# Kernel optimization log

Hardware: AMD Instinct MI355X
Metric: run time of the kernel (lower is better)

Reference implementation:

```python
import jax, jax.numpy as jnp
import numpy as np

B, S, D, H = 2, 2048, 1024, 16
DEPTH = D // H


def setup_inputs() -> dict:
    key = jax.random.key(0)
    ks = jax.random.split(key, 6)
    q = jax.random.normal(ks[0], (B, S, D), dtype=jnp.float32)
    k = jax.random.normal(ks[1], (B, S, D), dtype=jnp.float32)
    v = jax.random.normal(ks[2], (B, S, D), dtype=jnp.float32)
    # causal mask, broadcastable to [B, H, S, S]
    mask = jnp.tril(jnp.ones((S, S), dtype=bool))[None, None, :, :]
    wq = jax.random.normal(ks[3], (D, D), dtype=jnp.float32)
    wk = jax.random.normal(ks[4], (D, D), dtype=jnp.float32)
    wv = jax.random.normal(ks[5], (D, D), dtype=jnp.float32)
    return {"q": q, "k": k, "v": v, "mask": mask, "wq": wq, "wk": wk, "wv": wv}


def _split_heads(x):
    # [B, S, D] -> [B, H, S, depth]
    return x.reshape(x.shape[0], -1, H, DEPTH).transpose(0, 2, 1, 3)


def reference(q, k, v, mask, wq, wk, wv):
    q = _split_heads(q @ wq)
    k = _split_heads(k @ wk)
    v = _split_heads(v @ wv)
    scale = jnp.sqrt(jnp.float32(DEPTH))
    # [B, H, S, S]
    scores = jnp.einsum("bhqd,bhkd->bhqk", q, k) / scale
    scores = jnp.where(mask, scores, jnp.float32(-8.0))
    scores = scores - jnp.max(scores, axis=-1, keepdims=True)
    attn = jax.nn.softmax(scores, axis=-1)
    out = jnp.einsum("bhqk,bhkd->bhqd", attn, v)
    # [B, H, S, depth] -> [B, S, D]
    return out.transpose(0, 2, 1, 3).reshape(out.shape[0], -1, D)
```

## Files before the change

kernel.cpp:

```cpp
#include <hip/hip_runtime.h>
#include <hip/hip_bf16.h>

#define B_  2
#define S_  2048
#define D_  1024
#define H_  16
#define DH_ 64

typedef __attribute__((ext_vector_type(8)))  short  short8;
typedef __attribute__((ext_vector_type(4)))  short  short4b;
typedef __attribute__((ext_vector_type(16))) float  f32x16;

#define MFMA32(A,B,C) __builtin_amdgcn_mfma_f32_32x32x16_bf16(A,B,C,0,0,0)

static __device__ __forceinline__ short bf16b(float x) {
    __hip_bfloat16 h = __float2bfloat16(x);
    return *(short*)&h;
}
static __device__ __forceinline__ float bf16tof(short s) {
    union { unsigned u; float f; } cv;
    cv.u = ((unsigned)(unsigned short)s) << 16;
    return cv.f;
}
static __device__ __forceinline__ void gl2lds(const short* g, short* l) {
    __builtin_amdgcn_global_load_lds(
        (const __attribute__((address_space(1))) unsigned int*)g,
        (__attribute__((address_space(3))) unsigned int*)l, 16, 0, 0);
}

__global__ __launch_bounds__(256)
void conv_x(const float* __restrict__ q, const float* __restrict__ k,
            const float* __restrict__ v, char* __restrict__ ws) {
    const int z = blockIdx.y;
    const float* src = z == 0 ? q : z == 1 ? k : v;
    short* hi = (short*)(ws + (size_t)z * 16777216);
    short* lo = hi + 4194304;
    const int i = (blockIdx.x * 256 + threadIdx.x) * 4;
    float4 xv = *(const float4*)&src[i];
    const float* xf = (const float*)&xv;
    short4b h4, l4;
#pragma unroll
    for (int e = 0; e < 4; ++e) {
        short hb = bf16b(xf[e]);
        h4[e] = hb;
        l4[e] = bf16b(xf[e] - bf16tof(hb));
    }
    *(short4b*)&hi[i] = h4;
    *(short4b*)&lo[i] = l4;
}

__global__ __launch_bounds__(256)
void conv_wT(const float* __restrict__ wq, const float* __restrict__ wk,
             const float* __restrict__ wv, char* __restrict__ ws) {
    __shared__ short HiT[64][80];
    __shared__ short LoT[64][80];
    const int z = blockIdx.z;
    const float* w = z == 0 ? wq : z == 1 ? wk : wv;
    short* oh = (short*)(ws + 50331648 + (size_t)z * 4194304);
    short* ol = oh + 1048576;
    const int t  = threadIdx.x;
    const int k0 = blockIdx.x * 64, n0 = blockIdx.y * 64;

    const int kr = t >> 2, c4 = (t & 3) * 16;
    const float* srow = w + (size_t)(k0 + kr) * 1024 + n0 + c4;
#pragma unroll
    for (int u = 0; u < 16; u += 4) {
        float4 f = *(const float4*)&srow[u];
        const float* ff = (const float*)&f;
#pragma unroll
        for (int e = 0; e < 4; ++e) {
            int nl = c4 + u + e;
            short hb = bf16b(ff[e]);
            HiT[nl][kr] = hb;
            LoT[nl][kr] = bf16b(ff[e] - bf16tof(hb));
        }
    }
    __syncthreads();
    const int nl = t >> 2, kc = (t & 3) * 16;
    size_t off = (size_t)(n0 + nl) * 1024 + k0 + kc;
    *(short8*)&oh[off]     = *(const short8*)&HiT[nl][kc];
    *(short8*)&oh[off + 8] = *(const short8*)&HiT[nl][kc + 8];
    *(short8*)&ol[off]     = *(const short8*)&LoT[nl][kc];
    *(short8*)&ol[off + 8] = *(const short8*)&LoT[nl][kc + 8];
}

#define AHI_ 0
#define ALO_ 4096
#define BHI_ 8192
#define BLO_ 12288

__global__ __launch_bounds__(256, 2)
void proj_mfma(const short* __restrict__ xh0, const short* __restrict__ xl0,
               const short* __restrict__ xh1, const short* __restrict__ xl1,
               const short* __restrict__ xh2, const short* __restrict__ xl2,
               const short* __restrict__ wh0, const short* __restrict__ wl0,
               const short* __restrict__ wh1, const short* __restrict__ wl1,
               const short* __restrict__ wh2, const short* __restrict__ wl2,
               short* __restrict__ qh, short* __restrict__ ql,
               short* __restrict__ kh, short* __restrict__ kl,
               short* __restrict__ vt) {
    __shared__ short lds[16384];
    const int z  = blockIdx.z;
    const int m0 = blockIdx.y * 128;
    const int n0 = blockIdx.x * 128;
    const int t = threadIdx.x, lane = t & 63, w = t >> 6;
    const int l31 = lane & 31, hh = lane >> 5;

    const short* xh = z == 0 ? xh0 : z == 1 ? xh1 : xh2;
    const short* xl = z == 0 ? xl0 : z == 1 ? xl1 : xl2;
    const short* wh = z == 0 ? wh0 : z == 1 ? wh1 : wh2;
    const short* wl = z == 0 ? wl0 : z == 1 ? wl1 : wl2;

    const short* gsrc[8];
    short*       ldst[8];
#pragma unroll
    for (int j = 0; j < 8; ++j) {
        int sub = ((j & 1) << 2) | w;
        int cc  = (sub << 6) | lane;
        int row = cc >> 2, p = cc & 3;
        int kc  = p ^ ((row & 3) ^ ((row >> 2) & 3));
        bool isA  = j < 4;
        bool isHi = (j & 2) == 0;
        const short* base = isA ? (isHi ? xh : xl) : (isHi ? wh : wl);
        int r0g = isA ? m0 : n0;
        gsrc[j] = base + (size_t)(r0g + row) * 1024 + kc * 8;
        ldst[j] = &lds[(j >> 1) * 4096 + sub * 512];
    }

    const int rm0 = ((w & 1) << 6) + l31, rm1 = rm0 + 32;
    const int rn0 = ((w >> 1) << 6) + l31, rn1 = rn0 + 32;
    const int swm = (rm0 & 3) ^ ((rm0 >> 2) & 3);
    const int swn = (rn0 & 3) ^ ((rn0 >> 2) & 3);

    f32x16 accs[2][2] = {};

    for (int kt = 0; kt < 32; ++kt) {
        __syncthreads();
#pragma unroll
        for (int j = 0; j < 8; ++j)
            gl2lds(gsrc[j] + kt * 32, ldst[j]);
        __syncthreads();
#pragma unroll
        for (int ks = 0; ks < 2; ++ks) {
            const int kc = (ks << 1) | hh;
            const int om = (kc ^ swm) << 3;
            const int on = (kc ^ swn) << 3;
            short8 ah0 = *(const short8*)&lds[AHI_ + rm0 * 32 + om];
            short8 ah1 = *(const short8*)&lds[AHI_ + rm1 * 32 + om];
            short8 al0 = *(const short8*)&lds[ALO_ + rm0 * 32 + om];
            short8 al1 = *(const short8*)&lds[ALO_ + rm1 * 32 + om];
            short8 bh0 = *(const short8*)&lds[BHI_ + rn0 * 32 + on];
            short8 bh1 = *(const short8*)&lds[BHI_ + rn1 * 32 + on];
            short8 bl0 = *(const short8*)&lds[BLO_ + rn0 * 32 + on];
            short8 bl1 = *(const short8*)&lds[BLO_ + rn1 * 32 + on];
            accs[0][0] = MFMA32(ah0, bh0, accs[0][0]);
            accs[0][0] = MFMA32(ah0, bl0, accs[0][0]);
            accs[0][0] = MFMA32(al0, bh0, accs[0][0]);
            accs[0][1] = MFMA32(ah0, bh1, accs[0][1]);
            accs[0][1] = MFMA32(ah0, bl1, accs[0][1]);
            accs[0][1] = MFMA32(al0, bh1, accs[0][1]);
            accs[1][0] = MFMA32(ah1, bh0, accs[1][0]);
            accs[1][0] = MFMA32(ah1, bl0, accs[1][0]);
            accs[1][0] = MFMA32(al1, bh0, accs[1][0]);
            accs[1][1] = MFMA32(ah1, bh1, accs[1][1]);
            accs[1][1] = MFMA32(ah1, bl1, accs[1][1]);
            accs[1][1] = MFMA32(al1, bh1, accs[1][1]);
        }
    }

    const int qm = w & 1, qn = w >> 1;
    const int bb = m0 >> 11;
    const int sbase = (m0 & 2047) + qm * 64;
    if (z < 2) {
        short* oh = z == 0 ? qh : kh;
        short* ol = z == 0 ? ql : kl;
#pragma unroll
        for (int mt = 0; mt < 2; ++mt)
#pragma unroll
        for (int nt = 0; nt < 2; ++nt) {
            int n_g = n0 + qn * 64 + nt * 32 + l31;
            int h = n_g >> 6, d = n_g & 63;
#pragma unroll
            for (int r = 0; r < 16; ++r) {
                int s = sbase + mt * 32 + (r & 3) + 8 * (r >> 2) + 4 * hh;
                size_t off = (((size_t)(bb * 16 + h) * 2048 + s) << 6) + d;
                float a = accs[mt][nt][r];
                short hb = bf16b(a);
                oh[off] = hb;
                ol[off] = bf16b(a - bf16tof(hb));
            }
        }
    } else {
#pragma unroll
        for (int mt = 0; mt < 2; ++mt)
#pragma unroll
        for (int nt = 0; nt < 2; ++nt) {
            int n_g = n0 + qn * 64 + nt * 32 + l31;
            int h = n_g >> 6, d = n_g & 63;
            size_t vbase = ((size_t)(bb * 16 + h) * 64 + d) * 2048;
#pragma unroll
            for (int r2 = 0; r2 < 4; ++r2) {
                int s0 = sbase + mt * 32 + 8 * r2 + 4 * hh;
                short4b pk;
#pragma unroll
                for (int a2 = 0; a2 < 4; ++a2)
                    pk[a2] = bf16b(accs[mt][nt][r2 * 4 + a2]);
                *(short4b*)&vt[vbase + s0] = pk;
            }
        }
    }
}

__global__ void vtile_sums(const short* __restrict__ Vt, float* __restrict__ TS) {
    int c = blockIdx.x, bh = blockIdx.y, d = threadIdx.x;
    const short* row = Vt + ((size_t)bh * DH_ + d) * S_ + c * 64;
    float s = 0.f;
    for (int j = 0; j < 64; ++j) s += bf16tof(row[j]);
    TS[((size_t)bh * 32 + c) * 64 + d] = s;
}

__global__ void suffix_scan(const float* __restrict__ TS, float* __restrict__ SV) {
    int bh = blockIdx.x, d = threadIdx.x;
    float run = 0.f;
    for (int c = 32; c >= 0; --c) {
        SV[((size_t)bh * 33 + c) * 64 + d] = run;
        if (c > 0) run += TS[((size_t)bh * 32 + (c - 1)) * 64 + d];
    }
}

__global__ __launch_bounds__(256, 2)
void attn_mfma(const short* __restrict__ Qhi, const short* __restrict__ Qlo,
               const short* __restrict__ Khi, const short* __restrict__ Klo,
               const short* __restrict__ Vt,  const float* __restrict__ SV,
               float* __restrict__ out) {
    __shared__ __align__(16) short KhiS[64 * 72];
    __shared__ __align__(16) short KloS[64 * 72];
    __shared__ __align__(16) short VtS [64 * 72];
    __shared__ __align__(16) short PS  [4][32 * 72];

    const int t     = threadIdx.x;
    const int lane  = t & 63;
    const int w     = t >> 6;
    const int l31   = lane & 31;
    const int hh    = lane >> 5;
    const int bh    = blockIdx.x;
    const int yy    = blockIdx.y;
    const int qt    = (yy < 8) ? yy : 23 - yy;
    const int q0    = qt * 128;
    const int myq   = q0 + w * 32 + l31;
    const int ktend = 2 * qt + 2;

    const size_t basebh = (size_t)bh * S_ * DH_;

    short8 qh[4], ql[4];
    {
        const short* qr = Qhi + basebh + (size_t)myq * DH_;
        const short* lr = Qlo + basebh + (size_t)myq * DH_;
#pragma unroll
        for (int kf = 0; kf < 4; ++kf) {
            int dofs = kf * 16 + hh * 8;
            qh[kf] = *(const short8*)(qr + dofs);
            ql[kf] = *(const short8*)(lr + dofs);
        }
    }

    float m_run = -INFINITY, l_run = 0.f;
    f32x16 oT0 = {}, oT1 = {};

    const int srow = t >> 2;
    const int sc16 = (t & 3) * 16;

    for (int kt = 0; kt < ktend; ++kt) {
        __syncthreads();
        {
            const short* gH = Khi + basebh + (size_t)(kt * 64 + srow) * 64 + sc16;
            const short* gL = Klo + basebh + (size_t)(kt * 64 + srow) * 64 + sc16;
            const short* gV = Vt + (size_t)bh * DH_ * S_ + (size_t)srow * S_ + kt * 64 + sc16;
            short8 a0 = *(const short8*)gH, a1 = *(const short8*)(gH + 8);
            short8 b0 = *(const short8*)gL, b1 = *(const short8*)(gL + 8);
            short8 c0 = *(const short8*)gV, c1 = *(const short8*)(gV + 8);
            *(short8*)&KhiS[srow * 72 + sc16]     = a0;
            *(short8*)&KhiS[srow * 72 + sc16 + 8] = a1;
            *(short8*)&KloS[srow * 72 + sc16]     = b0;
            *(short8*)&KloS[srow * 72 + sc16 + 8] = b1;
            *(short8*)&VtS [srow * 72 + sc16]     = c0;
            *(short8*)&VtS [srow * 72 + sc16 + 8] = c1;
        }
        __syncthreads();

        f32x16 acc0 = {}, acc1 = {};
#pragma unroll
        for (int kf = 0; kf < 4; ++kf) {
            int dofs = kf * 16 + hh * 8;
            short8 k0h = *(const short8*)&KhiS[(l31)      * 72 + dofs];
            short8 k0l = *(const short8*)&KloS[(l31)      * 72 + dofs];
            short8 k1h = *(const short8*)&KhiS[(l31 + 32) * 72 + dofs];
            short8 k1l = *(const short8*)&KloS[(l31 + 32) * 72 + dofs];
            acc0 = MFMA32(k0h, qh[kf], acc0);
            acc0 = MFMA32(k0h, ql[kf], acc0);
            acc0 = MFMA32(k0l, qh[kf], acc0);
            acc1 = MFMA32(k1h, qh[kf], acc1);
            acc1 = MFMA32(k1h, ql[kf], acc1);
            acc1 = MFMA32(k1l, qh[kf], acc1);
        }

        float vals[32];
        float tmax = -INFINITY;
#pragma unroll
        for (int r = 0; r < 16; ++r) {
            int key0 = kt * 64 + ((r & 3) + 8 * (r >> 2) + 4 * hh);
            float v0 = acc0[r] * 0.125f;
            v0 = (key0 <= myq) ? v0 : -8.0f;
            float v1 = acc1[r] * 0.125f;
            v1 = (key0 + 32 <= myq) ? v1 : -8.0f;
            vals[r] = v0;
            vals[16 + r] = v1;
            tmax = fmaxf(tmax, fmaxf(v0, v1));
        }
        tmax = fmaxf(tmax, __shfl_xor(tmax, 32, 64));
        float mnew  = fmaxf(m_run, tmax);
        float alpha = __expf(m_run - mnew);
        float psum  = 0.f;
#pragma unroll
        for (int mt = 0; mt < 2; ++mt)
#pragma unroll
            for (int b2 = 0; b2 < 4; ++b2) {
                short4b pk;
#pragma unroll
                for (int a = 0; a < 4; ++a) {
                    float p = __expf(vals[mt * 16 + b2 * 4 + a] - mnew);
                    short pb = bf16b(p);
                    psum += bf16tof(pb);
                    pk[a] = pb;
                }
                *(short4b*)&PS[w][l31 * 72 + mt * 32 + b2 * 8 + hh * 4] = pk;
            }
        psum += __shfl_xor(psum, 32, 64);
        l_run = l_run * alpha + psum;
        m_run = mnew;
#pragma unroll
        for (int r = 0; r < 16; ++r) { oT0[r] *= alpha; oT1[r] *= alpha; }

#pragma unroll
        for (int kf = 0; kf < 4; ++kf) {
            int kofs = kf * 16 + hh * 8;
            short8 pf = *(const short8*)&PS[w][l31 * 72 + kofs];
            short8 v0 = *(const short8*)&VtS[(l31)      * 72 + kofs];
            short8 v1 = *(const short8*)&VtS[(l31 + 32) * 72 + kofs];
            oT0 = MFMA32(v0, pf, oT0);
            oT1 = MFMA32(v1, pf, oT1);
        }
    }

    {
        float mfin = fmaxf(m_run, -8.0f);
        float aa   = __expf(m_run - mfin);
        float e8   = __expf(-8.0f - mfin);
        float nrem = (float)(S_ - ktend * 64);
        float lfin = l_run * aa + nrem * e8;
        float inv  = 1.0f / lfin;
        const float* sv = SV + ((size_t)bh * 33 + ktend) * 64;
#pragma unroll
        for (int r = 0; r < 16; ++r) {
            int dim0 = (r & 3) + 8 * (r >> 2) + 4 * hh;
            oT0[r] = (oT0[r] * aa + e8 * sv[dim0])      * inv;
            oT1[r] = (oT1[r] * aa + e8 * sv[dim0 + 32]) * inv;
        }
    }

    __syncthreads();
    float* Ob = (w == 0) ? (float*)KhiS :
                (w == 1) ? (float*)KloS :
                (w == 2) ? (float*)VtS  : (float*)PS;
#pragma unroll
    for (int r = 0; r < 16; ++r) {
        int dim0 = (r & 3) + 8 * (r >> 2) + 4 * hh;
        Ob[l31 * 68 + dim0]      = oT0[r];
        Ob[l31 * 68 + dim0 + 32] = oT1[r];
    }
    {
        const int qq = lane >> 1;
        const int ch = (lane & 1) * 32;
        const float* src = Ob + qq * 68 + ch;
        const int b  = bh >> 4;
        const int h  = bh & 15;
        float* dst = out + ((size_t)b * S_ + (q0 + w * 32 + qq)) * D_ + h * 64 + ch;
#pragma unroll
        for (int c = 0; c < 32; c += 4)
            *(float4*)(dst + c) = *(const float4*)(src + c);
    }
}

extern "C" void kernel_launch(void* const* d_in, const int* in_sizes, int n_in,
                              void* d_out, int out_size, void* d_ws, size_t ws_size,
                              hipStream_t stream) {
    const float* q  = (const float*)d_in[0];
    const float* k  = (const float*)d_in[1];
    const float* v  = (const float*)d_in[2];
    const float* wq = (const float*)d_in[4];
    const float* wk = (const float*)d_in[5];
    const float* wv = (const float*)d_in[6];
    float* out = (float*)d_out;

    char* ws = (char*)d_ws;
    const short* XH[3] = {(short*)ws, (short*)(ws + 16777216), (short*)(ws + 33554432)};
    const short* XL[3] = {XH[0] + 4194304, XH[1] + 4194304, XH[2] + 4194304};
    const short* WH[3] = {(short*)(ws + 50331648), (short*)(ws + 54525952), (short*)(ws + 58720256)};
    const short* WL[3] = {WH[0] + 1048576, WH[1] + 1048576, WH[2] + 1048576};
    float* TS = (float*)(ws + 62914560);
    float* SV = (float*)(ws + 62914560 + 262144);

    short* Qhi = (short*)d_in[0]; short* Qlo = Qhi + 4194304;
    short* Khi = (short*)d_in[1]; short* Klo = Khi + 4194304;
    short* Vt  = (short*)d_in[2];

    conv_x <<<dim3(4096, 3), 256, 0, stream>>>(q, k, v, ws);
    conv_wT<<<dim3(16, 16, 3), 256, 0, stream>>>(wq, wk, wv, ws);

    proj_mfma<<<dim3(8, 32, 3), 256, 0, stream>>>(
        XH[0], XL[0], XH[1], XL[1], XH[2], XL[2],
        WH[0], WL[0], WH[1], WL[1], WH[2], WL[2],
        Qhi, Qlo, Khi, Klo, Vt);

    vtile_sums<<<dim3(32, 32), 64, 0, stream>>>(Vt, TS);
    suffix_scan<<<32, 64, 0, stream>>>(TS, SV);

    attn_mfma<<<dim3(32, 16), 256, 0, stream>>>(Qhi, Qlo, Khi, Klo, Vt, SV, out);
}
```

Measured before the change: 294.0 us.

## Enlarge projection GEMM tiles to 256x256 with double-buffered LDS and MFMA priority

Reworks the split-bf16 projection GEMM so each 512-thread block computes a 256x256 output tile instead of 128x128, which raises operand reuse per LDS load. It double-buffers the K-loop in 128KB of LDS, prefetching the next K slice while MFMAs run on the current one. It also wraps MFMA groups in s_barrier/setprio to interleave waves. The costs are much higher LDS and register use per block and a grid of only 192 blocks, which may underfill the CUs.

```diff
diff --git a/kernel.cpp b/kernel.cpp
--- a/kernel.cpp
+++ b/kernel.cpp
@@ -84,12 +84,7 @@
     *(short8*)&ol[off + 8] = *(const short8*)&LoT[nl][kc + 8];
 }
 
-#define AHI_ 0
-#define ALO_ 4096
-#define BHI_ 8192
-#define BLO_ 12288
-
-__global__ __launch_bounds__(256, 2)
+__global__ __launch_bounds__(512, 2)
 void proj_mfma(const short* __restrict__ xh0, const short* __restrict__ xl0,
                const short* __restrict__ xh1, const short* __restrict__ xl1,
                const short* __restrict__ xh2, const short* __restrict__ xl2,
@@ -99,92 +94,108 @@
                short* __restrict__ qh, short* __restrict__ ql,
                short* __restrict__ kh, short* __restrict__ kl,
                short* __restrict__ vt) {
-    __shared__ short lds[16384];
+    __shared__ __align__(16) short lds[65536];
     const int z  = blockIdx.z;
-    const int m0 = blockIdx.y * 128;
-    const int n0 = blockIdx.x * 128;
+    const int m0 = blockIdx.y * 256;
+    const int n0 = blockIdx.x * 256;
     const int t = threadIdx.x, lane = t & 63, w = t >> 6;
     const int l31 = lane & 31, hh = lane >> 5;
+    const int wr = w >> 2, wc = w & 3;
 
     const short* xh = z == 0 ? xh0 : z == 1 ? xh1 : xh2;
     const short* xl = z == 0 ? xl0 : z == 1 ? xl1 : xl2;
     const short* wh = z == 0 ? wh0 : z == 1 ? wh1 : wh2;
     const short* wl = z == 0 ? wl0 : z == 1 ? wl1 : wl2;
 
-    const short* gsrc[8];
-    short*       ldst[8];
-#pragma unroll
-    for (int j = 0; j < 8; ++j) {
-        int sub = ((j & 1) << 2) | w;
-        int cc  = (sub << 6) | lane;
-        int row = cc >> 2, p = cc & 3;
-        int kc  = p ^ ((row & 3) ^ ((row >> 2) & 3));
-        bool isA  = j < 4;
-        bool isHi = (j & 2) == 0;
-        const short* base = isA ? (isHi ? xh : xl) : (isHi ? wh : wl);
-        int r0g = isA ? m0 : n0;
-        gsrc[j] = base + (size_t)(r0g + row) * 1024 + kc * 8;
-        ldst[j] = &lds[(j >> 1) * 4096 + sub * 512];
-    }
-
-    const int rm0 = ((w & 1) << 6) + l31, rm1 = rm0 + 32;
-    const int rn0 = ((w >> 1) << 6) + l31, rn1 = rn0 + 32;
-    const int swm = (rm0 & 3) ^ ((rm0 >> 2) & 3);
-    const int swn = (rn0 & 3) ^ ((rn0 >> 2) & 3);
-
-    f32x16 accs[2][2] = {};
+    const int cc   = (w << 6) | lane;
+    const int rowA = cc >> 2;
+    const int kcA  = (cc & 3) ^ ((rowA & 3) ^ ((rowA >> 2) & 3));
+    const size_t goff = (size_t)rowA * 1024 + (size_t)(kcA * 8);
+    const short* pA  = xh + (size_t)m0 * 1024 + goff;
+    const short* pAl = xl + (size_t)m0 * 1024 + goff;
+    const short* pB  = wh + (size_t)n0 * 1024 + goff;
+    const short* pBl = wl + (size_t)n0 * 1024 + goff;
+
+#define STAGE(KT, BOF) do {                                                   \
+        const int ko_ = (KT) * 32;                                            \
+        short* Ld_ = &lds[(BOF) + w * 512];                                   \
+        gl2lds(pA  + ko_,          Ld_);               \
+        gl2lds(pA  + ko_ + 131072, Ld_ + 4096);        \
+        gl2lds(pAl + ko_,          Ld_ + 8192);                               \
+        gl2lds(pAl + ko_ + 131072, Ld_ + 12288);                              \
+        gl2lds(pB  + ko_,          Ld_ + 16384);                              \
+        gl2lds(pB  + ko_ + 131072, Ld_ + 20480);                              \
+        gl2lds(pBl + ko_,          Ld_ + 24576);                              \
+        gl2lds(pBl + ko_ + 131072, Ld_ + 28672);                              \
+    } while (0)
+
+    const int swl = (l31 & 3) ^ ((l31 >> 2) & 3);
+    const int c0  = (hh ^ swl) << 3;
+    const int c1  = (((2 + hh)) ^ swl) << 3;
+
+    f32x16 acc[4][2] = {};
+
+    STAGE(0, 0);
+    __syncthreads();
 
     for (int kt = 0; kt < 32; ++kt) {
+        const int cb = (kt & 1) << 15;
+        if (kt < 31) STAGE(kt + 1, ((kt & 1) ^ 1) << 15);
+
+        short8 bh_[2][2], bl_[2][2];
+#pragma unroll
+        for (int j = 0; j < 2; ++j) {
+            const int rB = cb + 16384 + (wc * 64 + j * 32 + l31) * 32;
+            bh_[j][0] = *(const short8*)&lds[rB + c0];
+            bh_[j][1] = *(const short8*)&lds[rB + c1];
+            bl_[j][0] = *(const short8*)&lds[rB + 8192 + c0];
+            bl_[j][1] = *(const short8*)&lds[rB + 8192 + c1];
+        }
+#pragma unroll
+        for (int p = 0; p < 4; ++p) {
+            const int rA = cb + (wr * 128 + p * 32 + l31) * 32;
+            short8 ah0 = *(const short8*)&lds[rA + c0];
+            short8 ah1 = *(const short8*)&lds[rA + c1];
+            short8 al0 = *(const short8*)&lds[rA + 8192 + c0];
+            short8 al1 = *(const short8*)&lds[rA + 8192 + c1];
+            __builtin_amdgcn_s_barrier();
+            __builtin_amdgcn_s_setprio(1);
+            acc[p][0] = MFMA32(ah0, bh_[0][0], acc[p][0]);
+            acc[p][1] = MFMA32(ah0, bh_[1][0], acc[p][1]);
+            acc[p][0] = MFMA32(ah0, bl_[0][0], acc[p][0]);
+            acc[p][1] = MFMA32(ah0, bl_[1][0], acc[p][1]);
+            acc[p][0] = MFMA32(al0, bh_[0][0], acc[p][0]);
+            acc[p][1] = MFMA32(al0, bh_[1][0], acc[p][1]);
+            acc[p][0] = MFMA32(ah1, bh_[0][1], acc[p][0]);
+            acc[p][1] = MFMA32(ah1, bh_[1][1], acc[p][1]);
+            acc[p][0] = MFMA32(ah1, bl_[0][1], acc[p][0]);
+            acc[p][1] = MFMA32(ah1, bl_[1][1], acc[p][1]);
+            acc[p][0] = MFMA32(al1, bh_[0][1], acc[p][0]);
+            acc[p][1] = MFMA32(al1, bh_[1][1], acc[p][1]);
+            __builtin_amdgcn_s_setprio(0);
+            __builtin_amdgcn_s_barrier();
+            __builtin_amdgcn_sched_barrier(0);
+        }
         __syncthreads();
-#pragma unroll
-        for (int j = 0; j < 8; ++j)
-            gl2lds(gsrc[j] + kt * 32, ldst[j]);
-        __syncthreads();
-#pragma unroll
-        for (int ks = 0; ks < 2; ++ks) {
-            const int kc = (ks << 1) | hh;
-            const int om = (kc ^ swm) << 3;
-            const int on = (kc ^ swn) << 3;
-            short8 ah0 = *(const short8*)&lds[AHI_ + rm0 * 32 + om];
-            short8 ah1 = *(const short8*)&lds[AHI_ + rm1 * 32 + om];
-            short8 al0 = *(const short8*)&lds[ALO_ + rm0 * 32 + om];
-            short8 al1 = *(const short8*)&lds[ALO_ + rm1 * 32 + om];
-            short8 bh0 = *(const short8*)&lds[BHI_ + rn0 * 32 + on];
-            short8 bh1 = *(const short8*)&lds[BHI_ + rn1 * 32 + on];
-            short8 bl0 = *(const short8*)&lds[BLO_ + rn0 * 32 + on];
-            short8 bl1 = *(const short8*)&lds[BLO_ + rn1 * 32 + on];
-            accs[0][0] = MFMA32(ah0, bh0, accs[0][0]);
-            accs[0][0] = MFMA32(ah0, bl0, accs[0][0]);
-            accs[0][0] = MFMA32(al0, bh0, accs[0][0]);
-            accs[0][1] = MFMA32(ah0, bh1, accs[0][1]);
-            accs[0][1] = MFMA32(ah0, bl1, accs[0][1]);
-            accs[0][1] = MFMA32(al0, bh1, accs[0][1]);
-            accs[1][0] = MFMA32(ah1, bh0, accs[1][0]);
-            accs[1][0] = MFMA32(ah1, bl0, accs[1][0]);
-            accs[1][0] = MFMA32(al1, bh0, accs[1][0]);
-            accs[1][1] = MFMA32(ah1, bh1, accs[1][1]);
-            accs[1][1] = MFMA32(ah1, bl1, accs[1][1]);
-            accs[1][1] = MFMA32(al1, bh1, accs[1][1]);
-        }
-    }
-
-    const int qm = w & 1, qn = w >> 1;
-    const int bb = m0 >> 11;
-    const int sbase = (m0 & 2047) + qm * 64;
+    }
+#undef STAGE
+
+    const int bb  = m0 >> 11;
+    const int sb0 = (m0 & 2047) + wr * 128;
     if (z < 2) {
         short* oh = z == 0 ? qh : kh;
         short* ol = z == 0 ? ql : kl;
 #pragma unroll
-        for (int mt = 0; mt < 2; ++mt)
-#pragma unroll
-        for (int nt = 0; nt < 2; ++nt) {
-            int n_g = n0 + qn * 64 + nt * 32 + l31;
-            int h = n_g >> 6, d = n_g & 63;
+        for (int i = 0; i < 4; ++i)
+#pragma unroll
+        for (int j = 0; j < 2; ++j) {
+            const int n_g = n0 + wc * 64 + j * 32 + l31;
+            const int h = n_g >> 6, d = n_g & 63;
 #pragma unroll
             for (int r = 0; r < 16; ++r) {
-                int s = sbase + mt * 32 + (r & 3) + 8 * (r >> 2) + 4 * hh;
-                size_t off = (((size_t)(bb * 16 + h) * 2048 + s) << 6) + d;
-                float a = accs[mt][nt][r];
+                const int s = sb0 + i * 32 + (r & 3) + 8 * (r >> 2) + 4 * hh;
+                const size_t off = (((size_t)(bb * 16 + h) * 2048 + s) << 6) + d;
+                float a = acc[i][j][r];
                 short hb = bf16b(a);
                 oh[off] = hb;
                 ol[off] = bf16b(a - bf16tof(hb));
@@ -192,19 +203,19 @@
         }
     } else {
 #pragma unroll
-        for (int mt = 0; mt < 2; ++mt)
-#pragma unroll
-        for (int nt = 0; nt < 2; ++nt) {
-            int n_g = n0 + qn * 64 + nt * 32 + l31;
-            int h = n_g >> 6, d = n_g & 63;
-            size_t vbase = ((size_t)(bb * 16 + h) * 64 + d) * 2048;
+        for (int i = 0; i < 4; ++i)
+#pragma unroll
+        for (int j = 0; j < 2; ++j) {
+            const int n_g = n0 + wc * 64 + j * 32 + l31;
+            const int h = n_g >> 6, d = n_g & 63;
+            const size_t vbase = ((size_t)(bb * 16 + h) * 64 + d) * 2048;
 #pragma unroll
             for (int r2 = 0; r2 < 4; ++r2) {
-                int s0 = sbase + mt * 32 + 8 * r2 + 4 * hh;
+                const int s0 = sb0 + i * 32 + 8 * r2 + 4 * hh;
                 short4b pk;
 #pragma unroll
                 for (int a2 = 0; a2 < 4; ++a2)
-                    pk[a2] = bf16b(accs[mt][nt][r2 * 4 + a2]);
+                    pk[a2] = bf16b(acc[i][j][r2 * 4 + a2]);
                 *(short4b*)&vt[vbase + s0] = pk;
             }
         }
@@ -417,7 +428,7 @@
     conv_x <<<dim3(4096, 3), 256, 0, stream>>>(q, k, v, ws);
     conv_wT<<<dim3(16, 16, 3), 256, 0, stream>>>(wq, wk, wv, ws);
 
-    proj_mfma<<<dim3(8, 32, 3), 256, 0, stream>>>(
+    proj_mfma<<<dim3(4, 16, 3), 512, 0, stream>>>(
         XH[0], XL[0], XH[1], XL[1], XH[2], XL[2],
         WH[0], WL[0], WH[1], WL[1], WH[2], WL[2],
         Qhi, Qlo, Khi, Klo, Vt);
```

After: 286.8 us. 2.4% less time.
